# Kernel optimization log

Hardware: AMD Instinct MI355X
Metric: run time of the kernel (lower is better)

Reference implementation:

```python
import jax, jax.numpy as jnp
import numpy as np

DIM = 1024
H = 16
HD = DIM // H  # 64
K = 256


def setup_inputs() -> dict:
    key = jax.random.key(0)
    ks = jax.random.split(key, 8)
    x = jax.random.normal(ks[0], (4, 4096, DIM), dtype=jnp.float32)
    # torch nn.Linear weights are (out, in); y = x @ W.T
    Wq = jax.random.normal(ks[1], (DIM, DIM), dtype=jnp.float32) * (DIM ** -0.5)
    Wk = jax.random.normal(ks[2], (DIM, DIM), dtype=jnp.float32) * (DIM ** -0.5)
    Wv = jax.random.normal(ks[3], (DIM, DIM), dtype=jnp.float32) * (DIM ** -0.5)
    E = jax.random.normal(ks[4], (K, HD), dtype=jnp.float32)
    F = jax.random.normal(ks[5], (K, HD), dtype=jnp.float32)
    Wo = jax.random.normal(ks[6], (DIM, DIM), dtype=jnp.float32) * (DIM ** -0.5)
    bo = jax.random.normal(ks[7], (DIM,), dtype=jnp.float32) * 0.01
    return {"x": x, "Wq": Wq, "Wk": Wk, "Wv": Wv, "E": E, "F": F, "Wo": Wo, "bo": bo}


def reference(x, Wq, Wk, Wv, E, F, Wo, bo):
    B, N, D = x.shape
    d = HD
    q = (x @ Wq.T).reshape(B, N, H, d).transpose(0, 2, 1, 3)  # (B,H,N,d)
    k = (x @ Wk.T).reshape(B, N, H, d).transpose(0, 2, 1, 3)
    v = (x @ Wv.T).reshape(B, N, H, d).transpose(0, 2, 1, 3)
    # Faithful to source: einsum contracts over n (sequence), elementwise in d.
    k_proj = jnp.einsum('bhnd,kd->bhkd', k, E)  # (B,H,K,d)
    v_proj = jnp.einsum('bhnd,kd->bhkd', v, F)
    attn = jnp.einsum('bhnd,bhkd->bhnk', q, k_proj) / (d ** 0.5)  # (B,H,N,K)
    attn = jax.nn.softmax(attn, axis=-1)
    out = jnp.einsum('bhnk,bhkd->bhnd', attn, v_proj)
    out = out.transpose(0, 2, 1, 3).reshape(B, N, D)
    return out @ Wo.T + bo
```

## Files before the change

kernel.cpp:

```cpp
#include <hip/hip_runtime.h>

#define DIM 1024
#define BATCH 4
#define SEQ 4096
#define NH 16
#define HD 64
#define KP 256

typedef float f32x4 __attribute__((ext_vector_type(4)));
typedef _Float16 half8 __attribute__((ext_vector_type(8)));

__device__ __forceinline__ void gll16(const void* g, void* l) {
  __builtin_amdgcn_global_load_lds(
      (const __attribute__((address_space(1))) void*)g,
      (__attribute__((address_space(3))) void*)l, 16, 0, 0);
}

__global__ void k_cvt(const float* __restrict__ s, _Float16* __restrict__ d) {
  int i = (blockIdx.x * 256 + threadIdx.x) * 8;
  f32x4 a = *(const f32x4*)(s + i);
  f32x4 b = *(const f32x4*)(s + i + 4);
  half8 h;
  h[0] = a[0]; h[1] = a[1]; h[2] = a[2]; h[3] = a[3];
  h[4] = b[0]; h[5] = b[1]; h[6] = b[2]; h[7] = b[3];
  *(half8*)(d + i) = h;
}

__global__ void k_zero(float* p) { p[blockIdx.x * 256 + threadIdx.x] = 0.f; }

__global__ void k_xsum(const float* __restrict__ x, float* __restrict__ xs) {
  int c = blockIdx.x * 256 + threadIdx.x;
  int b = blockIdx.y;
  int n0 = blockIdx.z * 128;
  const float* p = x + (size_t)(b * SEQ + n0) * DIM + c;
  float s = 0.f;
  #pragma unroll 8
  for (int i = 0; i < 128; i++) s += p[i * DIM];
  atomicAdd(&xs[b * DIM + c], s);
}

__global__ void k_sksv(const float* __restrict__ xs, const float* __restrict__ Wk,
                       const float* __restrict__ Wv, float* __restrict__ Sk,
                       float* __restrict__ Sv) {
  int idx = blockIdx.x * 4 + (threadIdx.x >> 6);
  int lane = threadIdx.x & 63;
  int kv = idx >> 12;
  int rem = idx & 4095;
  int b = rem >> 10, c = rem & 1023;
  const float* W = (kv ? Wv : Wk) + c * DIM;
  const float* xp = xs + b * DIM;
  float a = 0.f;
  #pragma unroll
  for (int i = 0; i < 16; i++) a += xp[lane + i * 64] * W[lane + i * 64];
  for (int off = 32; off; off >>= 1) a += __shfl_down(a, off);
  if (lane == 0) (kv ? Sv : Sk)[rem] = a;
}

__global__ void k_ft(const float* __restrict__ F, _Float16* __restrict__ Ft) {
  int i = blockIdx.x * 256 + threadIdx.x;
  int k = i >> 6, d = i & 63;
  Ft[d * KP + (k & 15) * 16 + (k >> 4)] = (_Float16)F[i];
}

template <int MODE>
__global__ __launch_bounds__(256) void k_gemm(const _Float16* __restrict__ A,
                                              const _Float16* __restrict__ Bw,
                                              void* __restrict__ Cout,
                                              const float* __restrict__ sb) {
  __shared__ _Float16 As[128 * 32];
  __shared__ _Float16 Bs[128 * 32];
  const int tid = threadIdx.x;
  const int w = tid >> 6, lane = tid & 63;
  const int m0 = blockIdx.x * 128, n0 = blockIdx.y * 128;
  const int q4 = lane >> 4, mm = lane & 15;
  const int wm = w & 1, wn = w >> 1;
  f32x4 acc[4][4] = {};
  const _Float16* Ag = A + (m0 + w * 32 + (lane >> 2)) * DIM + (lane & 3) * 8;
  const _Float16* Bg = Bw + (n0 + w * 32 + (lane >> 2)) * DIM + (lane & 3) * 8;
  _Float16* AsW = As + w * 1024;
  _Float16* BsW = Bs + w * 1024;
  for (int k0 = 0; k0 < DIM; k0 += 32) {
    gll16(Ag + k0, AsW);
    gll16(Ag + k0 + 16 * DIM, AsW + 512);
    gll16(Bg + k0, BsW);
    gll16(Bg + k0 + 16 * DIM, BsW + 512);
    __syncthreads();
    half8 av[4], bv[4];
    const _Float16* Ap = As + (wm * 64 + mm) * 32 + q4 * 8;
    const _Float16* Bp = Bs + (wn * 64 + mm) * 32 + q4 * 8;
    #pragma unroll
    for (int t = 0; t < 4; t++) {
      av[t] = *(const half8*)(Ap + t * 512);
      bv[t] = *(const half8*)(Bp + t * 512);
    }
    #pragma unroll
    for (int mt = 0; mt < 4; mt++)
      #pragma unroll
      for (int nt = 0; nt < 4; nt++)
        acc[mt][nt] = __builtin_amdgcn_mfma_f32_16x16x32_f16(av[mt], bv[nt], acc[mt][nt], 0, 0, 0);
    __syncthreads();
  }
  const int bIdx = m0 >> 12;
  #pragma unroll
  for (int nt = 0; nt < 4; nt++) {
    int colg = n0 + wn * 64 + nt * 16 + mm;
    float s = (MODE == 0) ? sb[bIdx * DIM + colg] * (0.125f * 1.44269504088896f)
                          : sb[colg];
    #pragma unroll
    for (int mt = 0; mt < 4; mt++) {
      int rowg = m0 + wm * 64 + mt * 16 + q4 * 4;
      #pragma unroll
      for (int r = 0; r < 4; r++) {
        float v = acc[mt][nt][r];
        if (MODE == 0)
          ((_Float16*)Cout)[(rowg + r) * DIM + colg] = (_Float16)(v * s);
        else
          ((float*)Cout)[(rowg + r) * DIM + colg] = v + s;
      }
    }
  }
}

__global__ __launch_bounds__(256, 1) void k_attn(const _Float16* __restrict__ Q,
                                                 const _Float16* __restrict__ E,
                                                 const _Float16* __restrict__ Ftp,
                                                 const float* __restrict__ Sv,
                                                 _Float16* __restrict__ O) {
  __shared__ _Float16 Ps[4][16][264];
  const int tid = threadIdx.x;
  const int w = tid >> 6, lane = tid & 63;
  const int q4 = lane >> 4, mm = lane & 15;
  const int bh = blockIdx.y;
  const int b = bh >> 4, h = bh & 15;
  const int row_base = blockIdx.x * 1024 + w * 256;

  half8 ef[16][2];
  #pragma unroll
  for (int t = 0; t < 16; t++)
    #pragma unroll
    for (int kk = 0; kk < 2; kk++)
      ef[t][kk] = *(const half8*)(E + (t * 16 + mm) * HD + kk * 32 + q4 * 8);
  half8 ff[4][8];
  #pragma unroll
  for (int nt = 0; nt < 4; nt++)
    #pragma unroll
    for (int kk = 0; kk < 8; kk++)
      ff[nt][kk] = *(const half8*)(Ftp + (nt * 16 + mm) * KP + kk * 32 + q4 * 8);
  float sv[4];
  #pragma unroll
  for (int nt = 0; nt < 4; nt++) sv[nt] = Sv[b * DIM + h * HD + nt * 16 + mm];

  const _Float16* Qbase = Q + ((size_t)(b * SEQ + row_base + mm)) * DIM + h * HD + q4 * 8;
  half8 qa0 = *(const half8*)(Qbase);
  half8 qa1 = *(const half8*)(Qbase + 32);

  for (int tile = 0; tile < 16; tile++) {
    f32x4 acc[16] = {};
    #pragma unroll
    for (int t = 0; t < 16; t++)
      acc[t] = __builtin_amdgcn_mfma_f32_16x16x32_f16(qa0, ef[t][0], acc[t], 0, 0, 0);
    #pragma unroll
    for (int t = 0; t < 16; t++)
      acc[t] = __builtin_amdgcn_mfma_f32_16x16x32_f16(qa1, ef[t][1], acc[t], 0, 0, 0);
    half8 qn0, qn1;
    if (tile < 15) {
      const _Float16* Qn = Qbase + (size_t)(tile + 1) * 16 * DIM;
      qn0 = *(const half8*)(Qn);
      qn1 = *(const half8*)(Qn + 32);
    }
    float mx[4] = {-1e30f, -1e30f, -1e30f, -1e30f};
    #pragma unroll
    for (int t = 0; t < 16; t++)
      #pragma unroll
      for (int r = 0; r < 4; r++) mx[r] = fmaxf(mx[r], acc[t][r]);
    #pragma unroll
    for (int r = 0; r < 4; r++)
      for (int msk = 1; msk < 16; msk <<= 1) mx[r] = fmaxf(mx[r], __shfl_xor(mx[r], msk));
    float sm[4] = {0.f, 0.f, 0.f, 0.f};
    #pragma unroll
    for (int t = 0; t < 16; t++)
      #pragma unroll
      for (int r = 0; r < 4; r++) {
        float p = __builtin_amdgcn_exp2f(acc[t][r] - mx[r]);
        acc[t][r] = p;
        sm[r] += p;
      }
    #pragma unroll
    for (int r = 0; r < 4; r++) {
      for (int msk = 1; msk < 16; msk <<= 1) sm[r] += __shfl_xor(sm[r], msk);
      sm[r] = 1.f / sm[r];
    }
    #pragma unroll
    for (int r = 0; r < 4; r++) {
      half8 h0, h1;
      #pragma unroll
      for (int t = 0; t < 8; t++) h0[t] = (_Float16)(acc[t][r] * sm[r]);
      #pragma unroll
      for (int t = 0; t < 8; t++) h1[t] = (_Float16)(acc[t + 8][r] * sm[r]);
      *(half8*)&Ps[w][q4 * 4 + r][mm * 16] = h0;
      *(half8*)&Ps[w][q4 * 4 + r][mm * 16 + 8] = h1;
    }
    f32x4 acc2[4] = {};
    #pragma unroll
    for (int kk = 0; kk < 8; kk++) {
      half8 pa = *(const half8*)&Ps[w][mm][kk * 32 + q4 * 8];
      #pragma unroll
      for (int nt = 0; nt < 4; nt++)
        acc2[nt] = __builtin_amdgcn_mfma_f32_16x16x32_f16(pa, ff[nt][kk], acc2[nt], 0, 0, 0);
    }
    const int rw0 = row_base + tile * 16;
    #pragma unroll
    for (int nt = 0; nt < 4; nt++)
      #pragma unroll
      for (int r = 0; r < 4; r++)
        O[(size_t)(b * SEQ + rw0 + q4 * 4 + r) * DIM + h * HD + nt * 16 + mm] =
            (_Float16)(acc2[nt][r] * sv[nt]);
    qa0 = qn0;
    qa1 = qn1;
  }
}

extern "C" void kernel_launch(void* const* d_in, const int* in_sizes, int n_in,
                              void* d_out, int out_size, void* d_ws, size_t ws_size,
                              hipStream_t stream) {
  (void)in_sizes; (void)n_in; (void)out_size; (void)ws_size;
  const float* x  = (const float*)d_in[0];
  const float* Wq = (const float*)d_in[1];
  const float* Wk = (const float*)d_in[2];
  const float* Wv = (const float*)d_in[3];
  const float* E  = (const float*)d_in[4];
  const float* F  = (const float*)d_in[5];
  const float* Wo = (const float*)d_in[6];
  const float* bo = (const float*)d_in[7];
  char* ws = (char*)d_ws;
  _Float16* x_h  = (_Float16*)(ws);
  _Float16* O_h  = (_Float16*)(ws);
  _Float16* Q_h  = (_Float16*)(ws + 33554432);
  _Float16* Wq_h = (_Float16*)(ws + 67108864);
  _Float16* Wo_h = (_Float16*)(ws + 69206016);
  _Float16* E_h  = (_Float16*)(ws + 71303168);
  _Float16* Ft_h = (_Float16*)(ws + 71335936);
  float* xsum    = (float*)(ws + 71368704);
  float* Sk      = (float*)(ws + 71385088);
  float* Sv      = (float*)(ws + 71401472);
  float* out     = (float*)d_out;

  k_zero<<<16, 256, 0, stream>>>(xsum);
  k_xsum<<<dim3(4, BATCH, 32), 256, 0, stream>>>(x, xsum);
  k_cvt<<<8192, 256, 0, stream>>>(x, x_h);
  k_cvt<<<512, 256, 0, stream>>>(Wq, Wq_h);
  k_cvt<<<512, 256, 0, stream>>>(Wo, Wo_h);
  k_cvt<<<8, 256, 0, stream>>>(E, E_h);
  k_ft<<<64, 256, 0, stream>>>(F, Ft_h);
  k_sksv<<<2048, 256, 0, stream>>>(xsum, Wk, Wv, Sk, Sv);
  k_gemm<0><<<dim3(128, 8), 256, 0, stream>>>(x_h, Wq_h, (void*)Q_h, Sk);
  k_attn<<<dim3(4, 64), 256, 0, stream>>>(Q_h, E_h, Ft_h, Sv, O_h);
  k_gemm<1><<<dim3(128, 8), 256, 0, stream>>>(O_h, Wo_h, (void*)out, bo);
}
```

Measured before the change: 315.7 us.

## Merge small prep kernels, sum x in fp16, relayout GEMM LDS, widen attention grid

Several setup kernels (zero, E convert, F transpose, and the two weight conversions) are merged into two launches to cut launch overhead. The x column-sum now reads the fp16 copy of x, halving the bytes it reads, though it loses some precision. The GEMM global-to-LDS load pattern and its fragment reads are relaid out, which changes LDS access patterns and bank behaviour. Attention now launches 4x more blocks with fewer rows each and drops the one-block-per-CU launch bound, trading more redundant loading of the E/F fragments for better occupancy.

```diff
diff --git a/kernel.cpp b/kernel.cpp
--- a/kernel.cpp
+++ b/kernel.cpp
@@ -26,16 +26,49 @@
   *(half8*)(d + i) = h;
 }
 
-__global__ void k_zero(float* p) { p[blockIdx.x * 256 + threadIdx.x] = 0.f; }
-
-__global__ void k_xsum(const float* __restrict__ x, float* __restrict__ xs) {
+__global__ void k_cvtw(const float* __restrict__ Wq, const float* __restrict__ Wo,
+                       _Float16* __restrict__ Wq_h, _Float16* __restrict__ Wo_h) {
+  int bb = blockIdx.x;
+  const float* s = (bb < 512) ? Wq : Wo;
+  _Float16* d = (bb < 512) ? Wq_h : Wo_h;
+  int i = ((bb & 511) * 256 + threadIdx.x) * 8;
+  f32x4 a = *(const f32x4*)(s + i);
+  f32x4 b = *(const f32x4*)(s + i + 4);
+  half8 h;
+  h[0] = a[0]; h[1] = a[1]; h[2] = a[2]; h[3] = a[3];
+  h[4] = b[0]; h[5] = b[1]; h[6] = b[2]; h[7] = b[3];
+  *(half8*)(d + i) = h;
+}
+
+__global__ void k_misc(const float* __restrict__ E, const float* __restrict__ F,
+                       _Float16* __restrict__ E_h, _Float16* __restrict__ Ft,
+                       float* __restrict__ xsum) {
+  int bb = blockIdx.x;
+  if (bb < 16) {
+    xsum[bb * 256 + threadIdx.x] = 0.f;
+  } else if (bb < 24) {
+    int i = ((bb - 16) * 256 + threadIdx.x) * 8;
+    f32x4 a = *(const f32x4*)(E + i);
+    f32x4 b = *(const f32x4*)(E + i + 4);
+    half8 h;
+    h[0] = a[0]; h[1] = a[1]; h[2] = a[2]; h[3] = a[3];
+    h[4] = b[0]; h[5] = b[1]; h[6] = b[2]; h[7] = b[3];
+    *(half8*)(E_h + i) = h;
+  } else {
+    int i = (bb - 24) * 256 + threadIdx.x;
+    int k = i >> 6, d = i & 63;
+    Ft[d * KP + (k & 15) * 16 + (k >> 4)] = (_Float16)F[i];
+  }
+}
+
+__global__ void k_xsum(const _Float16* __restrict__ xh, float* __restrict__ xs) {
   int c = blockIdx.x * 256 + threadIdx.x;
   int b = blockIdx.y;
   int n0 = blockIdx.z * 128;
-  const float* p = x + (size_t)(b * SEQ + n0) * DIM + c;
+  const _Float16* p = xh + (size_t)(b * SEQ + n0) * DIM + c;
   float s = 0.f;
   #pragma unroll 8
-  for (int i = 0; i < 128; i++) s += p[i * DIM];
+  for (int i = 0; i < 128; i++) s += (float)p[i * DIM];
   atomicAdd(&xs[b * DIM + c], s);
 }
 
@@ -54,12 +87,6 @@
   for (int i = 0; i < 16; i++) a += xp[lane + i * 64] * W[lane + i * 64];
   for (int off = 32; off; off >>= 1) a += __shfl_down(a, off);
   if (lane == 0) (kv ? Sv : Sk)[rem] = a;
-}
-
-__global__ void k_ft(const float* __restrict__ F, _Float16* __restrict__ Ft) {
-  int i = blockIdx.x * 256 + threadIdx.x;
-  int k = i >> 6, d = i & 63;
-  Ft[d * KP + (k & 15) * 16 + (k >> 4)] = (_Float16)F[i];
 }
 
 template <int MODE>
@@ -75,23 +102,23 @@
   const int q4 = lane >> 4, mm = lane & 15;
   const int wm = w & 1, wn = w >> 1;
   f32x4 acc[4][4] = {};
-  const _Float16* Ag = A + (m0 + w * 32 + (lane >> 2)) * DIM + (lane & 3) * 8;
-  const _Float16* Bg = Bw + (n0 + w * 32 + (lane >> 2)) * DIM + (lane & 3) * 8;
+  const _Float16* Ag = A + (m0 + w * 32 + (lane & 31)) * DIM + (lane >> 5) * 8;
+  const _Float16* Bg = Bw + (n0 + w * 32 + (lane & 31)) * DIM + (lane >> 5) * 8;
   _Float16* AsW = As + w * 1024;
   _Float16* BsW = Bs + w * 1024;
   for (int k0 = 0; k0 < DIM; k0 += 32) {
     gll16(Ag + k0, AsW);
-    gll16(Ag + k0 + 16 * DIM, AsW + 512);
+    gll16(Ag + k0 + 16, AsW + 512);
     gll16(Bg + k0, BsW);
-    gll16(Bg + k0 + 16 * DIM, BsW + 512);
+    gll16(Bg + k0 + 16, BsW + 512);
     __syncthreads();
     half8 av[4], bv[4];
-    const _Float16* Ap = As + (wm * 64 + mm) * 32 + q4 * 8;
-    const _Float16* Bp = Bs + (wn * 64 + mm) * 32 + q4 * 8;
     #pragma unroll
     for (int t = 0; t < 4; t++) {
-      av[t] = *(const half8*)(Ap + t * 512);
-      bv[t] = *(const half8*)(Bp + t * 512);
+      av[t] = *(const half8*)(As + (wm * 2 + (t >> 1)) * 1024 + q4 * 256 +
+                              ((t & 1) * 16 + mm) * 8);
+      bv[t] = *(const half8*)(Bs + (wn * 2 + (t >> 1)) * 1024 + q4 * 256 +
+                              ((t & 1) * 16 + mm) * 8);
     }
     #pragma unroll
     for (int mt = 0; mt < 4; mt++)
@@ -121,18 +148,18 @@
   }
 }
 
-__global__ __launch_bounds__(256, 1) void k_attn(const _Float16* __restrict__ Q,
-                                                 const _Float16* __restrict__ E,
-                                                 const _Float16* __restrict__ Ftp,
-                                                 const float* __restrict__ Sv,
-                                                 _Float16* __restrict__ O) {
+__global__ __launch_bounds__(256) void k_attn(const _Float16* __restrict__ Q,
+                                              const _Float16* __restrict__ E,
+                                              const _Float16* __restrict__ Ftp,
+                                              const float* __restrict__ Sv,
+                                              _Float16* __restrict__ O) {
   __shared__ _Float16 Ps[4][16][264];
   const int tid = threadIdx.x;
   const int w = tid >> 6, lane = tid & 63;
   const int q4 = lane >> 4, mm = lane & 15;
   const int bh = blockIdx.y;
   const int b = bh >> 4, h = bh & 15;
-  const int row_base = blockIdx.x * 1024 + w * 256;
+  const int row_base = blockIdx.x * 256 + w * 64;
 
   half8 ef[16][2];
   #pragma unroll
@@ -154,7 +181,7 @@
   half8 qa0 = *(const half8*)(Qbase);
   half8 qa1 = *(const half8*)(Qbase + 32);
 
-  for (int tile = 0; tile < 16; tile++) {
+  for (int tile = 0; tile < 4; tile++) {
     f32x4 acc[16] = {};
     #pragma unroll
     for (int t = 0; t < 16; t++)
@@ -163,7 +190,7 @@
     for (int t = 0; t < 16; t++)
       acc[t] = __builtin_amdgcn_mfma_f32_16x16x32_f16(qa1, ef[t][1], acc[t], 0, 0, 0);
     half8 qn0, qn1;
-    if (tile < 15) {
+    if (tile < 3) {
       const _Float16* Qn = Qbase + (size_t)(tile + 1) * 16 * DIM;
       qn0 = *(const half8*)(Qn);
       qn1 = *(const half8*)(Qn + 32);
@@ -245,15 +272,12 @@
   float* Sv      = (float*)(ws + 71401472);
   float* out     = (float*)d_out;
 
-  k_zero<<<16, 256, 0, stream>>>(xsum);
-  k_xsum<<<dim3(4, BATCH, 32), 256, 0, stream>>>(x, xsum);
   k_cvt<<<8192, 256, 0, stream>>>(x, x_h);
-  k_cvt<<<512, 256, 0, stream>>>(Wq, Wq_h);
-  k_cvt<<<512, 256, 0, stream>>>(Wo, Wo_h);
-  k_cvt<<<8, 256, 0, stream>>>(E, E_h);
-  k_ft<<<64, 256, 0, stream>>>(F, Ft_h);
+  k_misc<<<88, 256, 0, stream>>>(E, F, E_h, Ft_h, xsum);
+  k_cvtw<<<1024, 256, 0, stream>>>(Wq, Wo, Wq_h, Wo_h);
+  k_xsum<<<dim3(4, BATCH, 32), 256, 0, stream>>>(x_h, xsum);
   k_sksv<<<2048, 256, 0, stream>>>(xsum, Wk, Wv, Sk, Sv);
   k_gemm<0><<<dim3(128, 8), 256, 0, stream>>>(x_h, Wq_h, (void*)Q_h, Sk);
-  k_attn<<<dim3(4, 64), 256, 0, stream>>>(Q_h, E_h, Ft_h, Sv, O_h);
+  k_attn<<<dim3(16, 64), 256, 0, stream>>>(Q_h, E_h, Ft_h, Sv, O_h);
   k_gemm<1><<<dim3(128, 8), 256, 0, stream>>>(O_h, Wo_h, (void*)out, bo);
 }
```

Result: slower. 368.5 us (+16.7%).
